# Kernel optimization log

Hardware: AMD Instinct MI355X
Metric: run time of the kernel (lower is better)

The kernel has to match this reference:

```python
import jax, jax.numpy as jnp
import numpy as np

N_NODES = 100000
N_EDGES = 1600000
D = 128
NUM_LAYERS = 3
BN_EPS = 1e-5


def setup_inputs() -> dict:
    key = jax.random.key(0)
    k1, k2, k3 = jax.random.split(key, 3)
    x = jax.random.normal(k1, (N_NODES, D), dtype=jnp.float32)
    edge_index = jax.random.randint(k2, (2, N_EDGES), 0, N_NODES, dtype=jnp.int32)
    # xavier-uniform-ish scale for relu gain
    scale = jnp.sqrt(2.0) * jnp.sqrt(6.0 / (D + D))
    Ws = jax.random.uniform(k3, (NUM_LAYERS, D, D), dtype=jnp.float32, minval=-1.0, maxval=1.0) * scale
    gammas = jnp.ones((NUM_LAYERS - 1, D), dtype=jnp.float32)
    betas = jnp.zeros((NUM_LAYERS - 1, D), dtype=jnp.float32)
    return {"x": x, "edge_index": edge_index, "Ws": Ws, "gammas": gammas, "betas": betas}


def gcn_conv(x, W, src, dst, num_nodes):
    # GCNConv(normalize=False, bias=False): linear then scatter-add aggregation
    h = x @ W                               # [N, D]
    msgs = h[src]                           # [E, D] irregular gather
    return jax.ops.segment_sum(msgs, dst, num_segments=num_nodes)  # [N, D] scatter-add


def batch_norm(x, gamma, beta):
    # training-mode BN over node dim, biased variance (torch semantics), deterministic
    mu = jnp.mean(x, axis=0)
    var = jnp.var(x, axis=0)
    return (x - mu) * jax.lax.rsqrt(var + BN_EPS) * gamma + beta


def reference(x, edge_index, Ws, gammas, betas):
    src, dst = edge_index[0], edge_index[1]
    n = x.shape[0]
    for i in range(NUM_LAYERS):
        x = gcn_conv(x, Ws[i], src, dst, n)
        if i != NUM_LAYERS - 1:
            x = batch_norm(x, gammas[i], betas[i])
            x = jax.nn.relu(x)
            # dropout omitted for a deterministic reference (eval-equivalent)
    return jax.nn.log_softmax(x, axis=-1)
```

## Files before the change

kernel.cpp:

```cpp
#include <hip/hip_runtime.h>

#define BN_EPS 1e-5f

typedef __attribute__((ext_vector_type(8))) short bf16x8;
typedef __attribute__((ext_vector_type(4))) float f32x4;

union VU {
    uint4 u;
    bf16x8 b;
};


__global__ __launch_bounds__(256) void hist_k(const int* __restrict__ dst, int E,
                                              int* __restrict__ ghist, int NB) {
    __shared__ int lh[128];
    if (threadIdx.x < 128) lh[threadIdx.x] = 0;
    __syncthreads();
    for (int i = blockIdx.x * 256 + threadIdx.x; i < E; i += gridDim.x * 256)
        atomicAdd(&lh[dst[i] >> 10], 1);
    __syncthreads();
    if (threadIdx.x < 128 && threadIdx.x < NB && lh[threadIdx.x])
        atomicAdd(&ghist[threadIdx.x * 16], lh[threadIdx.x]);
}

__global__ __launch_bounds__(128) void pscan_k(const int* __restrict__ ghist, int NB,
                                               int* __restrict__ sbase, int* __restrict__ csrB,
                                               int* __restrict__ rowptr, int n, int E) {
    __shared__ int pa[128], pc[128];
    int t = threadIdx.x;
    int v = (t < NB) ? ghist[t * 16] : 0;
    int vp = (v + 15) & ~15;
    pa[t] = vp;
    pc[t] = v;
    __syncthreads();
    for (int s = 1; s < 128; s <<= 1) {
        int ta = (t >= s) ? pa[t - s] : 0;
        int tc = (t >= s) ? pc[t - s] : 0;
        __syncthreads();
        pa[t] += ta;
        pc[t] += tc;
        __syncthreads();
    }
    if (t < NB) {
        sbase[t] = pa[t] - vp;
        csrB[t] = pc[t] - v;
        if (t == NB - 1) {
            csrB[NB] = pc[t];
            rowptr[n] = E;
        }
    }
}

#define CHUNK 2048
__global__ __launch_bounds__(256) void bin_k(const int* __restrict__ src, const int* __restrict__ dst, int E,
                                             const int* __restrict__ sbase, int* __restrict__ snext,
                                             int* __restrict__ staged, int NB) {
    __shared__ int hist[128];
    __shared__ int base[128];
    int t = threadIdx.x;
    int c0 = blockIdx.x * CHUNK;
    if (c0 >= E) return;
    if (t < 128) hist[t] = 0;
    __syncthreads();
    int bk[8], pk[8], rk[8];
#pragma unroll
    for (int k = 0; k < 8; ++k) {
        int i = c0 + k * 256 + t;
        bk[k] = -1;
        if (i < E) {
            int d = dst[i];
            int b = d >> 10;
            bk[k] = b;
            pk[k] = src[i] | ((d & 1023) << 17);
            rk[k] = atomicAdd(&hist[b], 1);
        }
    }
    __syncthreads();
    if (t < NB) base[t] = sbase[t] + atomicAdd(&snext[t * 16], hist[t]);
    __syncthreads();
#pragma unroll
    for (int k = 0; k < 8; ++k)
        if (bk[k] >= 0) staged[base[bk[k]] + rk[k]] = pk[k];
}

__global__ __launch_bounds__(1024) void csr_k(const int* __restrict__ staged, const int* __restrict__ ghist,
                                              const int* __restrict__ sbase, const int* __restrict__ csrB,
                                              int* __restrict__ rowptr, int* __restrict__ ssrc, int n) {
    __shared__ int hist[1024], cur[1024];
    int b = blockIdx.x, t = threadIdx.x;
    int nodeBase = b << 10;
    hist[t] = 0;
    __syncthreads();
    int s0 = sbase[b], c = ghist[b * 16];
    for (int j = t; j < c; j += 1024) atomicAdd(&hist[staged[s0 + j] >> 17], 1);
    __syncthreads();
    int v = hist[t];
    for (int s = 1; s < 1024; s <<= 1) {
        int tv = (t >= s) ? hist[t - s] : 0;
        __syncthreads();
        hist[t] += tv;
        __syncthreads();
    }
    int ex = hist[t] - v;
    int cb = csrB[b];
    if (nodeBase + t < n) rowptr[nodeBase + t] = cb + ex;
    cur[t] = ex;
    __syncthreads();
    for (int j = t; j < c; j += 1024) {
        int e = staged[s0 + j];
        int p = atomicAdd(&cur[e >> 17], 1);
        ssrc[cb + p] = e & 131071;
    }
}


static __device__ __forceinline__ unsigned short f2bf(float f) {
    unsigned u = __float_as_uint(f);
    unsigned r = (u + 0x7FFFu + ((u >> 16) & 1u)) >> 16;
    return (unsigned short)r;
}
static __device__ __forceinline__ float bf_lo(unsigned u) { return __uint_as_float(u << 16); }
static __device__ __forceinline__ float bf_hi(unsigned u) { return __uint_as_float(u & 0xFFFF0000u); }


__global__ __launch_bounds__(256) void prepw_k(const float* __restrict__ Ws, uint4* __restrict__ Wp) {
    int id = blockIdx.x * 256 + threadIdx.x;
    if (id >= 3 * 4 * 8 * 64) return;
    int lane = id & 63;
    int nt = (id >> 6) & 7;
    int kt = (id >> 9) & 3;
    int L = id >> 11;
    int quad = lane >> 4, l16 = lane & 15;
    const float* wsrc = Ws + L * 16384 + (kt * 32 + quad * 8) * 128 + nt * 16 + l16;
    unsigned short s[8];
#pragma unroll
    for (int j = 0; j < 8; ++j) s[j] = f2bf(wsrc[j * 128]);
    uint4 pk;
    pk.x = (unsigned)s[0] | ((unsigned)s[1] << 16);
    pk.y = (unsigned)s[2] | ((unsigned)s[3] << 16);
    pk.z = (unsigned)s[4] | ((unsigned)s[5] << 16);
    pk.w = (unsigned)s[6] | ((unsigned)s[7] << 16);
    Wp[id] = pk;
}


template <int MODE>
__global__ __launch_bounds__(256) void mgemm_k(const float* __restrict__ Xf, const unsigned short* __restrict__ Xb,
                                               const uint4* __restrict__ Wp, unsigned short* __restrict__ H,
                                               const float* __restrict__ ss, int n) {
    int lane = threadIdx.x & 63;
    int quad = lane >> 4, l16 = lane & 15;
    int wid = (blockIdx.x * 256 + threadIdx.x) >> 6;
    int nw = (gridDim.x * 256) >> 6;
    int ntiles = (n + 15) >> 4;

    VU b[4][8];
#pragma unroll
    for (int kt = 0; kt < 4; ++kt)
#pragma unroll
        for (int nt = 0; nt < 8; ++nt) b[kt][nt].u = Wp[(kt * 8 + nt) * 64 + lane];

    auto loadA = [&](int tile, VU* a) {
        int row = tile * 16 + l16;
#pragma unroll
        for (int kt = 0; kt < 4; ++kt) {
            float f[8];
            if (MODE == 0) {
                const float* xr = Xf + (size_t)row * 128 + kt * 32 + quad * 8;
                float4 u0 = *(const float4*)(xr);
                float4 u1 = *(const float4*)(xr + 4);
                f[0] = u0.x; f[1] = u0.y; f[2] = u0.z; f[3] = u0.w;
                f[4] = u1.x; f[5] = u1.y; f[6] = u1.z; f[7] = u1.w;
            } else {
                int sl = kt * 2 + (quad >> 1);
                uint4 u = *(const uint4*)(Xb + ((size_t)sl * n + row) * 16 + (quad & 1) * 8);
                f[0] = bf_lo(u.x); f[1] = bf_hi(u.x); f[2] = bf_lo(u.y); f[3] = bf_hi(u.y);
                f[4] = bf_lo(u.z); f[5] = bf_hi(u.z); f[6] = bf_lo(u.w); f[7] = bf_hi(u.w);
                const float4* scp = (const float4*)(ss + kt * 32 + quad * 8);
                const float4* shp = (const float4*)(ss + 128 + kt * 32 + quad * 8);
                float4 c0 = scp[0], c1 = scp[1], d0 = shp[0], d1 = shp[1];
                f[0] = fmaxf(fmaf(f[0], c0.x, d0.x), 0.f);
                f[1] = fmaxf(fmaf(f[1], c0.y, d0.y), 0.f);
                f[2] = fmaxf(fmaf(f[2], c0.z, d0.z), 0.f);
                f[3] = fmaxf(fmaf(f[3], c0.w, d0.w), 0.f);
                f[4] = fmaxf(fmaf(f[4], c1.x, d1.x), 0.f);
                f[5] = fmaxf(fmaf(f[5], c1.y, d1.y), 0.f);
                f[6] = fmaxf(fmaf(f[6], c1.z, d1.z), 0.f);
                f[7] = fmaxf(fmaf(f[7], c1.w, d1.w), 0.f);
            }
            uint4 pk;
            pk.x = (unsigned)f2bf(f[0]) | ((unsigned)f2bf(f[1]) << 16);
            pk.y = (unsigned)f2bf(f[2]) | ((unsigned)f2bf(f[3]) << 16);
            pk.z = (unsigned)f2bf(f[4]) | ((unsigned)f2bf(f[5]) << 16);
            pk.w = (unsigned)f2bf(f[6]) | ((unsigned)f2bf(f[7]) << 16);
            a[kt].u = pk;
        }
    };

    int t = wid;
    VU a[4];
    if (t < ntiles) loadA(t, a);

    while (t < ntiles) {
        int tn = t + nw;
        VU an[4];
        if (tn < ntiles) loadA(tn, an);

        f32x4 acc[8];
#pragma unroll
        for (int nt = 0; nt < 8; ++nt) acc[nt] = (f32x4){0.f, 0.f, 0.f, 0.f};
#pragma unroll
        for (int kt = 0; kt < 4; ++kt)
#pragma unroll
            for (int nt = 0; nt < 8; ++nt)
                acc[nt] = __builtin_amdgcn_mfma_f32_16x16x32_bf16(b[kt][nt].b, a[kt].b, acc[nt], 0, 0, 0);

        int row = t * 16 + l16;
#pragma unroll
        for (int nt = 0; nt < 8; ++nt) {
            uint2 pk;
            pk.x = (unsigned)f2bf(acc[nt][0]) | ((unsigned)f2bf(acc[nt][1]) << 16);
            pk.y = (unsigned)f2bf(acc[nt][2]) | ((unsigned)f2bf(acc[nt][3]) << 16);
            *(uint2*)(H + ((size_t)nt * n + row) * 16 + quad * 4) = pk;
        }

#pragma unroll
        for (int kt = 0; kt < 4; ++kt) a[kt] = an[kt];
        t = tn;
    }
}


template <int MODE>
__global__ __launch_bounds__(256) void aggs_k(const unsigned short* __restrict__ H, const int* __restrict__ rowptr,
                                              const int* __restrict__ ssrc, unsigned* __restrict__ outb,
                                              float* __restrict__ outf, float* __restrict__ stats, int n) {
    __shared__ float sred[4][4][8];
    int slice = blockIdx.x & 7;
    int bg = blockIdx.x >> 3;
    int lane = threadIdx.x & 63;
    int wv = threadIdx.x >> 6;
    int g = lane >> 3;
    int f = lane & 7;
    int wid = bg * 4 + wv;
    int nwave = (gridDim.x >> 3) * 4;
    const unsigned short* hs = H + (size_t)slice * n * 16 + f * 2;
    float s0 = 0, s1 = 0, q0 = 0, q1 = 0;

    for (int base = wid * 8; base < n; base += nwave * 8) {
        int node = base + g;
        bool valid = node < n;
        int cn = valid ? node : (n - 1);
        int beg = rowptr[cn];
        int end = valid ? rowptr[cn + 1] : beg;
        float ax = 0.f, ay = 0.f;

        for (int s = 0;; s += 16) {
            if (__ballot((beg + s) < end) == 0) break;
            int idx[16];
#pragma unroll
            for (int k = 0; k < 16; ++k) idx[k] = ssrc[beg + s + k];
            unsigned v[16];
#pragma unroll
            for (int k = 0; k < 16; ++k) v[k] = *(const unsigned*)(hs + (size_t)idx[k] * 16);
#pragma unroll
            for (int k = 0; k < 16; ++k) {
                float sc = (beg + s + k < end) ? 1.f : 0.f;
                ax = fmaf(sc, bf_lo(v[k]), ax);
                ay = fmaf(sc, bf_hi(v[k]), ay);
            }
        }

        if (MODE == 0) {
            if (valid) outb[((size_t)slice * n + node) * 8 + f] = (unsigned)f2bf(ax) | ((unsigned)f2bf(ay) << 16);
            s0 += ax; q0 += ax * ax;
            s1 += ay; q1 += ay * ay;
        } else {
            if (valid) *(float2*)(outf + (size_t)node * 128 + slice * 16 + f * 2) = make_float2(ax, ay);
        }
    }

    if (MODE == 0) {
        s0 += __shfl_xor(s0, 8); s0 += __shfl_xor(s0, 16); s0 += __shfl_xor(s0, 32);
        s1 += __shfl_xor(s1, 8); s1 += __shfl_xor(s1, 16); s1 += __shfl_xor(s1, 32);
        q0 += __shfl_xor(q0, 8); q0 += __shfl_xor(q0, 16); q0 += __shfl_xor(q0, 32);
        q1 += __shfl_xor(q1, 8); q1 += __shfl_xor(q1, 16); q1 += __shfl_xor(q1, 32);
        if (g == 0) {
            sred[wv][0][f] = s0;
            sred[wv][1][f] = s1;
            sred[wv][2][f] = q0;
            sred[wv][3][f] = q1;
        }
        __syncthreads();
        if (wv == 0 && g == 0) {
            float t0 = (sred[0][0][f] + sred[1][0][f]) + (sred[2][0][f] + sred[3][0][f]);
            float t1 = (sred[0][1][f] + sred[1][1][f]) + (sred[2][1][f] + sred[3][1][f]);
            float t2 = (sred[0][2][f] + sred[1][2][f]) + (sred[2][2][f] + sred[3][2][f]);
            float t3 = (sred[0][3][f] + sred[1][3][f]) + (sred[2][3][f] + sred[3][3][f]);
            atomicAdd(&stats[slice * 16 + 2 * f], t0);
            atomicAdd(&stats[slice * 16 + 2 * f + 1], t1);
            atomicAdd(&stats[128 + slice * 16 + 2 * f], t2);
            atomicAdd(&stats[128 + slice * 16 + 2 * f + 1], t3);
        }
    }
}


__global__ __launch_bounds__(256) void lsm_k(float* __restrict__ out, int n) {
    int lane = threadIdx.x & 63;
    int wid = (blockIdx.x * 256 + threadIdx.x) >> 6;
    int nw = (gridDim.x * 256) >> 6;
    for (int node = wid; node < n; node += nw) {
        float2 v = *(float2*)(out + (size_t)node * 128 + 2 * lane);
        float m = fmaxf(v.x, v.y);
#pragma unroll
        for (int off = 32; off > 0; off >>= 1) m = fmaxf(m, __shfl_xor(m, off));
        float ex = expf(v.x - m) + expf(v.y - m);
#pragma unroll
        for (int off = 32; off > 0; off >>= 1) ex += __shfl_xor(ex, off);
        float lse = m + logf(ex);
        *(float2*)(out + (size_t)node * 128 + 2 * lane) = make_float2(v.x - lse, v.y - lse);
    }
}


__global__ void bnfin_k(const float* __restrict__ stats, const float* __restrict__ gamma,
                        const float* __restrict__ beta, float* __restrict__ ss, int n) {
    int f = threadIdx.x;
    if (f < 128) {
        float mu = stats[f] / n;
        float var = stats[128 + f] / n - mu * mu;
        float rs = rsqrtf(fmaxf(var, 0.f) + BN_EPS);
        float sc = gamma[f] * rs;
        ss[f] = sc;
        ss[128 + f] = beta[f] - mu * sc;
    }
}


extern "C" void kernel_launch(void* const* d_in, const int* in_sizes, int n_in,
                              void* d_out, int out_size, void* d_ws, size_t ws_size,
                              hipStream_t stream) {
    const float* x = (const float*)d_in[0];
    const int* ei = (const int*)d_in[1];
    const float* Ws = (const float*)d_in[2];
    const float* gammas = (const float*)d_in[3];
    const float* betas = (const float*)d_in[4];
    int N = in_sizes[0] / 128;
    int E = in_sizes[1] / 2;
    const int* src = ei;
    const int* dst = ei + E;
    float* out = (float*)d_out;

    char* w = (char*)d_ws;
    size_t o = 0;
    auto alloc = [&](size_t bytes) { char* p = w + o; o += (bytes + 511) & ~511ull; return p; };
    unsigned short* h = (unsigned short*)alloc((size_t)N * 128 * 2);
    unsigned short* h2 = (unsigned short*)alloc((size_t)N * 128 * 2);
    int* rowptr = (int*)alloc(((size_t)N + 1) * 4);
    int* ssrc = (int*)alloc(((size_t)E + 256) * 4);
    uint4* Wp = (uint4*)alloc(3 * 2048 * 16);
    float* stats = (float*)alloc(512 * 4);
    float* ss = (float*)alloc(512 * 4);

    int NB = (N + 1023) >> 10;
    int* ghist = (int*)alloc((size_t)NB * 16 * 4);
    int* snext = (int*)alloc((size_t)NB * 16 * 4);
    int* sbase = (int*)alloc((size_t)NB * 4);
    int* csrB = (int*)alloc(((size_t)NB + 1) * 4);
    int* staged = (int*)h2;

    hipMemsetAsync(ghist, 0, (size_t)NB * 16 * 4, stream);
    hipMemsetAsync(snext, 0, (size_t)NB * 16 * 4, stream);
    hipMemsetAsync(stats, 0, 512 * 4, stream);
    hipMemsetAsync(ssrc + E, 0, 256 * 4, stream);

    prepw_k<<<24, 256, 0, stream>>>(Ws, Wp);
    hist_k<<<256, 256, 0, stream>>>(dst, E, ghist, NB);
    pscan_k<<<1, 128, 0, stream>>>(ghist, NB, sbase, csrB, rowptr, N, E);
    bin_k<<<(E + CHUNK - 1) / CHUNK, 256, 0, stream>>>(src, dst, E, sbase, snext, staged, NB);
    csr_k<<<NB, 1024, 0, stream>>>(staged, ghist, sbase, csrB, rowptr, ssrc, N);

    const int AGG_BLOCKS = 2048;
    const int GEMM_BLOCKS = 512;

    mgemm_k<0><<<GEMM_BLOCKS, 256, 0, stream>>>(x, nullptr, Wp, h, nullptr, N);
    aggs_k<0><<<AGG_BLOCKS, 256, 0, stream>>>(h, rowptr, ssrc, (unsigned*)h2, nullptr, stats, N);
    bnfin_k<<<1, 128, 0, stream>>>(stats, gammas, betas, ss, N);
    mgemm_k<1><<<GEMM_BLOCKS, 256, 0, stream>>>(nullptr, h2, Wp + 2048, h, ss, N);
    aggs_k<0><<<AGG_BLOCKS, 256, 0, stream>>>(h, rowptr, ssrc, (unsigned*)h2, nullptr, stats + 256, N);
    bnfin_k<<<1, 128, 0, stream>>>(stats + 256, gammas + 128, betas + 128, ss + 256, N);
    mgemm_k<1><<<GEMM_BLOCKS, 256, 0, stream>>>(nullptr, h2, Wp + 4096, h, ss + 256, N);
    aggs_k<1><<<AGG_BLOCKS, 256, 0, stream>>>(h, rowptr, ssrc, nullptr, out, nullptr, N);
    lsm_k<<<2048, 256, 0, stream>>>(out, N);
}
```

Baseline: 584.7 us.

## Switch node features to row-major layout with one wave per node in aggregation

Node features are now stored row-major (node × 128 bf16) instead of in 8 column slices of 16 features, and the GEMM loads and stores are updated to match. The aggregation kernel now gives each wave one whole node: every lane gathers one dword (2 features) per neighbor, so each neighbor fetch reads a full contiguous 256-byte row instead of eight 32-byte slice reads spread over separate passes. Neighbor indices are read once per node rather than once per slice, with the next batch of 8 indices prefetched. In exchange the graph is processed in one pass rather than 8 slice-local passes, so the per-slice cache locality is lost, and the gather depth per loop iteration drops to 8.

```diff
diff --git a/kernel.cpp b/kernel.cpp
--- a/kernel.cpp
+++ b/kernel.cpp
@@ -172,8 +172,7 @@
                 f[0] = u0.x; f[1] = u0.y; f[2] = u0.z; f[3] = u0.w;
                 f[4] = u1.x; f[5] = u1.y; f[6] = u1.z; f[7] = u1.w;
             } else {
-                int sl = kt * 2 + (quad >> 1);
-                uint4 u = *(const uint4*)(Xb + ((size_t)sl * n + row) * 16 + (quad & 1) * 8);
+                uint4 u = *(const uint4*)(Xb + (size_t)row * 128 + kt * 32 + quad * 8);
                 f[0] = bf_lo(u.x); f[1] = bf_hi(u.x); f[2] = bf_lo(u.y); f[3] = bf_hi(u.y);
                 f[4] = bf_lo(u.z); f[5] = bf_hi(u.z); f[6] = bf_lo(u.w); f[7] = bf_hi(u.w);
                 const float4* scp = (const float4*)(ss + kt * 32 + quad * 8);
@@ -221,7 +220,7 @@
             uint2 pk;
             pk.x = (unsigned)f2bf(acc[nt][0]) | ((unsigned)f2bf(acc[nt][1]) << 16);
             pk.y = (unsigned)f2bf(acc[nt][2]) | ((unsigned)f2bf(acc[nt][3]) << 16);
-            *(uint2*)(H + ((size_t)nt * n + row) * 16 + quad * 4) = pk;
+            *(uint2*)(H + (size_t)row * 128 + nt * 16 + quad * 4) = pk;
         }
 
 #pragma unroll
@@ -232,75 +231,67 @@
 
 
 template <int MODE>
-__global__ __launch_bounds__(256) void aggs_k(const unsigned short* __restrict__ H, const int* __restrict__ rowptr,
+__global__ __launch_bounds__(256) void aggr_k(const unsigned* __restrict__ Hdw, const int* __restrict__ rowptr,
                                               const int* __restrict__ ssrc, unsigned* __restrict__ outb,
                                               float* __restrict__ outf, float* __restrict__ stats, int n) {
-    __shared__ float sred[4][4][8];
-    int slice = blockIdx.x & 7;
-    int bg = blockIdx.x >> 3;
+    __shared__ float sred[4][4][64];
     int lane = threadIdx.x & 63;
     int wv = threadIdx.x >> 6;
-    int g = lane >> 3;
-    int f = lane & 7;
-    int wid = bg * 4 + wv;
-    int nwave = (gridDim.x >> 3) * 4;
-    const unsigned short* hs = H + (size_t)slice * n * 16 + f * 2;
-    float s0 = 0, s1 = 0, q0 = 0, q1 = 0;
-
-    for (int base = wid * 8; base < n; base += nwave * 8) {
-        int node = base + g;
-        bool valid = node < n;
-        int cn = valid ? node : (n - 1);
-        int beg = rowptr[cn];
-        int end = valid ? rowptr[cn + 1] : beg;
-        float ax = 0.f, ay = 0.f;
-
-        for (int s = 0;; s += 16) {
-            if (__ballot((beg + s) < end) == 0) break;
-            int idx[16];
-#pragma unroll
-            for (int k = 0; k < 16; ++k) idx[k] = ssrc[beg + s + k];
-            unsigned v[16];
-#pragma unroll
-            for (int k = 0; k < 16; ++k) v[k] = *(const unsigned*)(hs + (size_t)idx[k] * 16);
-#pragma unroll
-            for (int k = 0; k < 16; ++k) {
-                float sc = (beg + s + k < end) ? 1.f : 0.f;
-                ax = fmaf(sc, bf_lo(v[k]), ax);
-                ay = fmaf(sc, bf_hi(v[k]), ay);
+    int wid = blockIdx.x * 4 + wv;
+    int nwave = gridDim.x * 4;
+    float s0 = 0.f, s1 = 0.f, q0 = 0.f, q1 = 0.f;
+
+    for (int node = wid; node < n; node += nwave) {
+        int beg = __builtin_amdgcn_readfirstlane(rowptr[node]);
+        int end = __builtin_amdgcn_readfirstlane(rowptr[node + 1]);
+        int d = end - beg;
+        float a0 = 0.f, a1 = 0.f;
+
+        int idx[8];
+#pragma unroll
+        for (int k = 0; k < 8; ++k) idx[k] = ssrc[beg + k];
+
+        for (int s = 0; s < d; s += 8) {
+            int idn[8];
+#pragma unroll
+            for (int k = 0; k < 8; ++k) idn[k] = ssrc[beg + s + 8 + k];
+            unsigned v[8];
+#pragma unroll
+            for (int k = 0; k < 8; ++k) v[k] = Hdw[(size_t)(unsigned)idx[k] * 64 + lane];
+#pragma unroll
+            for (int k = 0; k < 8; ++k) {
+                float sc = (s + k < d) ? 1.f : 0.f;
+                a0 = fmaf(sc, bf_lo(v[k]), a0);
+                a1 = fmaf(sc, bf_hi(v[k]), a1);
             }
+#pragma unroll
+            for (int k = 0; k < 8; ++k) idx[k] = idn[k];
         }
 
         if (MODE == 0) {
-            if (valid) outb[((size_t)slice * n + node) * 8 + f] = (unsigned)f2bf(ax) | ((unsigned)f2bf(ay) << 16);
-            s0 += ax; q0 += ax * ax;
-            s1 += ay; q1 += ay * ay;
+            outb[(size_t)node * 64 + lane] = (unsigned)f2bf(a0) | ((unsigned)f2bf(a1) << 16);
+            s0 += a0; q0 += a0 * a0;
+            s1 += a1; q1 += a1 * a1;
         } else {
-            if (valid) *(float2*)(outf + (size_t)node * 128 + slice * 16 + f * 2) = make_float2(ax, ay);
+            *(float2*)(outf + (size_t)node * 128 + 2 * lane) = make_float2(a0, a1);
         }
     }
 
     if (MODE == 0) {
-        s0 += __shfl_xor(s0, 8); s0 += __shfl_xor(s0, 16); s0 += __shfl_xor(s0, 32);
-        s1 += __shfl_xor(s1, 8); s1 += __shfl_xor(s1, 16); s1 += __shfl_xor(s1, 32);
-        q0 += __shfl_xor(q0, 8); q0 += __shfl_xor(q0, 16); q0 += __shfl_xor(q0, 32);
-        q1 += __shfl_xor(q1, 8); q1 += __shfl_xor(q1, 16); q1 += __shfl_xor(q1, 32);
-        if (g == 0) {
-            sred[wv][0][f] = s0;
-            sred[wv][1][f] = s1;
-            sred[wv][2][f] = q0;
-            sred[wv][3][f] = q1;
-        }
-        __syncthreads();
-        if (wv == 0 && g == 0) {
-            float t0 = (sred[0][0][f] + sred[1][0][f]) + (sred[2][0][f] + sred[3][0][f]);
-            float t1 = (sred[0][1][f] + sred[1][1][f]) + (sred[2][1][f] + sred[3][1][f]);
-            float t2 = (sred[0][2][f] + sred[1][2][f]) + (sred[2][2][f] + sred[3][2][f]);
-            float t3 = (sred[0][3][f] + sred[1][3][f]) + (sred[2][3][f] + sred[3][3][f]);
-            atomicAdd(&stats[slice * 16 + 2 * f], t0);
-            atomicAdd(&stats[slice * 16 + 2 * f + 1], t1);
-            atomicAdd(&stats[128 + slice * 16 + 2 * f], t2);
-            atomicAdd(&stats[128 + slice * 16 + 2 * f + 1], t3);
+        sred[wv][0][lane] = s0;
+        sred[wv][1][lane] = s1;
+        sred[wv][2][lane] = q0;
+        sred[wv][3][lane] = q1;
+        __syncthreads();
+        if (wv == 0) {
+            float t0 = (sred[0][0][lane] + sred[1][0][lane]) + (sred[2][0][lane] + sred[3][0][lane]);
+            float t1 = (sred[0][1][lane] + sred[1][1][lane]) + (sred[2][1][lane] + sred[3][1][lane]);
+            float t2 = (sred[0][2][lane] + sred[1][2][lane]) + (sred[2][2][lane] + sred[3][2][lane]);
+            float t3 = (sred[0][3][lane] + sred[1][3][lane]) + (sred[2][3][lane] + sred[3][3][lane]);
+            atomicAdd(&stats[2 * lane], t0);
+            atomicAdd(&stats[2 * lane + 1], t1);
+            atomicAdd(&stats[128 + 2 * lane], t2);
+            atomicAdd(&stats[128 + 2 * lane + 1], t3);
         }
     }
 }
@@ -385,12 +376,12 @@
     const int GEMM_BLOCKS = 512;
 
     mgemm_k<0><<<GEMM_BLOCKS, 256, 0, stream>>>(x, nullptr, Wp, h, nullptr, N);
-    aggs_k<0><<<AGG_BLOCKS, 256, 0, stream>>>(h, rowptr, ssrc, (unsigned*)h2, nullptr, stats, N);
+    aggr_k<0><<<AGG_BLOCKS, 256, 0, stream>>>((const unsigned*)h, rowptr, ssrc, (unsigned*)h2, nullptr, stats, N);
     bnfin_k<<<1, 128, 0, stream>>>(stats, gammas, betas, ss, N);
     mgemm_k<1><<<GEMM_BLOCKS, 256, 0, stream>>>(nullptr, h2, Wp + 2048, h, ss, N);
-    aggs_k<0><<<AGG_BLOCKS, 256, 0, stream>>>(h, rowptr, ssrc, (unsigned*)h2, nullptr, stats + 256, N);
+    aggr_k<0><<<AGG_BLOCKS, 256, 0, stream>>>((const unsigned*)h, rowptr, ssrc, (unsigned*)h2, nullptr, stats + 256, N);
     bnfin_k<<<1, 128, 0, stream>>>(stats + 256, gammas + 128, betas + 128, ss + 256, N);
     mgemm_k<1><<<GEMM_BLOCKS, 256, 0, stream>>>(nullptr, h2, Wp + 4096, h, ss + 256, N);
-    aggs_k<1><<<AGG_BLOCKS, 256, 0, stream>>>(h, rowptr, ssrc, nullptr, out, nullptr, N);
+    aggr_k<1><<<AGG_BLOCKS, 256, 0, stream>>>((const unsigned*)h, rowptr, ssrc, nullptr, out, nullptr, N);
     lsm_k<<<2048, 256, 0, stream>>>(out, N);
 }
```

Result: slower. 601.4 us (+2.9%).

## Degree-sort nodes within buckets, software-pipeline gathers, fold memsets into prepw

Applied to the files above, without the earlier changes.

csr_k now counting-sorts each 1024-node bucket by in-degree (capped at 63) and writes an order permutation. The aggregation kernel processes nodes in that order, so the 8 nodes sharing a wave have similar degrees and less divergent padding work. The gather loop now runs a wave-uniform trip count in chunks of 8, with the next chunk's indices prefetched while the current one is summed. The four memsets are folded into prepw_k and the aggregation grid is set to 2000 blocks. The cost is an extra indirection load per node, and rows that read index padding past the last edge rely on the zeroed tail of ssrc.

```diff
diff --git a/kernel.cpp b/kernel.cpp
--- a/kernel.cpp
+++ b/kernel.cpp
@@ -85,11 +85,14 @@
 
 __global__ __launch_bounds__(1024) void csr_k(const int* __restrict__ staged, const int* __restrict__ ghist,
                                               const int* __restrict__ sbase, const int* __restrict__ csrB,
-                                              int* __restrict__ rowptr, int* __restrict__ ssrc, int n) {
+                                              int* __restrict__ rowptr, int* __restrict__ ssrc,
+                                              int* __restrict__ order, int n) {
     __shared__ int hist[1024], cur[1024];
+    __shared__ int dbin[64], dbs[64];
     int b = blockIdx.x, t = threadIdx.x;
     int nodeBase = b << 10;
     hist[t] = 0;
+    if (t < 64) dbin[t] = 0;
     __syncthreads();
     int s0 = sbase[b], c = ghist[b * 16];
     for (int j = t; j < c; j += 1024) atomicAdd(&hist[staged[s0 + j] >> 17], 1);
@@ -103,7 +106,8 @@
     }
     int ex = hist[t] - v;
     int cb = csrB[b];
-    if (nodeBase + t < n) rowptr[nodeBase + t] = cb + ex;
+    bool vn = (nodeBase + t) < n;
+    if (vn) rowptr[nodeBase + t] = cb + ex;
     cur[t] = ex;
     __syncthreads();
     for (int j = t; j < c; j += 1024) {
@@ -111,6 +115,24 @@
         int p = atomicAdd(&cur[e >> 17], 1);
         ssrc[cb + p] = e & 131071;
     }
+    int bin = 0, rk = 0;
+    if (vn) {
+        bin = min(v, 63);
+        rk = atomicAdd(&dbin[bin], 1);
+    }
+    __syncthreads();
+    if (t < 64) {
+        int cc = dbin[t];
+        int x = cc;
+#pragma unroll
+        for (int off = 1; off < 64; off <<= 1) {
+            int y = __shfl_up(x, off);
+            if (t >= off) x += y;
+        }
+        dbs[t] = x - cc;
+    }
+    __syncthreads();
+    if (vn) order[nodeBase + dbs[bin] + rk] = nodeBase + t;
 }
 
 
@@ -123,8 +145,14 @@
 static __device__ __forceinline__ float bf_hi(unsigned u) { return __uint_as_float(u & 0xFFFF0000u); }
 
 
-__global__ __launch_bounds__(256) void prepw_k(const float* __restrict__ Ws, uint4* __restrict__ Wp) {
+__global__ __launch_bounds__(256) void prepw_k(const float* __restrict__ Ws, uint4* __restrict__ Wp,
+                                               int* __restrict__ ghist, int* __restrict__ snext,
+                                               float* __restrict__ stats, int* __restrict__ ssrcPad, int NB16) {
     int id = blockIdx.x * 256 + threadIdx.x;
+    if (id < NB16) ghist[id] = 0;
+    else if (id < 2 * NB16) snext[id - NB16] = 0;
+    else if (id < 2 * NB16 + 512) stats[id - 2 * NB16] = 0.f;
+    else if (id < 2 * NB16 + 512 + 256) ssrcPad[id - 2 * NB16 - 512] = 0;
     if (id >= 3 * 4 * 8 * 64) return;
     int lane = id & 63;
     int nt = (id >> 6) & 7;
@@ -233,8 +261,9 @@
 
 template <int MODE>
 __global__ __launch_bounds__(256) void aggs_k(const unsigned short* __restrict__ H, const int* __restrict__ rowptr,
-                                              const int* __restrict__ ssrc, unsigned* __restrict__ outb,
-                                              float* __restrict__ outf, float* __restrict__ stats, int n) {
+                                              const int* __restrict__ ssrc, const int* __restrict__ order,
+                                              unsigned* __restrict__ outb, float* __restrict__ outf,
+                                              float* __restrict__ stats, int n) {
     __shared__ float sred[4][4][8];
     int slice = blockIdx.x & 7;
     int bg = blockIdx.x >> 3;
@@ -248,27 +277,39 @@
     float s0 = 0, s1 = 0, q0 = 0, q1 = 0;
 
     for (int base = wid * 8; base < n; base += nwave * 8) {
-        int node = base + g;
-        bool valid = node < n;
-        int cn = valid ? node : (n - 1);
-        int beg = rowptr[cn];
-        int end = valid ? rowptr[cn + 1] : beg;
+        bool valid = (base + g) < n;
+        int node = valid ? order[base + g] : 0;
+        int beg = rowptr[node];
+        int end = valid ? rowptr[node + 1] : beg;
         float ax = 0.f, ay = 0.f;
 
-        for (int s = 0;; s += 16) {
-            if (__ballot((beg + s) < end) == 0) break;
-            int idx[16];
-#pragma unroll
-            for (int k = 0; k < 16; ++k) idx[k] = ssrc[beg + s + k];
-            unsigned v[16];
-#pragma unroll
-            for (int k = 0; k < 16; ++k) v[k] = *(const unsigned*)(hs + (size_t)idx[k] * 16);
-#pragma unroll
-            for (int k = 0; k < 16; ++k) {
-                float sc = (beg + s + k < end) ? 1.f : 0.f;
+        int md = end - beg;
+        md = max(md, __shfl_xor(md, 8));
+        md = max(md, __shfl_xor(md, 16));
+        md = max(md, __shfl_xor(md, 32));
+        int nb = (md + 7) >> 3;
+
+        int idx[8];
+#pragma unroll
+        for (int k = 0; k < 8; ++k) idx[k] = ssrc[beg + k];
+
+        int j0 = beg;
+        for (int it = 0; it < nb; ++it) {
+            unsigned v[8];
+#pragma unroll
+            for (int k = 0; k < 8; ++k) v[k] = *(const unsigned*)(hs + (size_t)(unsigned)idx[k] * 16);
+            int idn[8];
+#pragma unroll
+            for (int k = 0; k < 8; ++k) idn[k] = ssrc[j0 + 8 + k];
+#pragma unroll
+            for (int k = 0; k < 8; ++k) {
+                float sc = (j0 + k < end) ? 1.f : 0.f;
                 ax = fmaf(sc, bf_lo(v[k]), ax);
                 ay = fmaf(sc, bf_hi(v[k]), ay);
             }
+#pragma unroll
+            for (int k = 0; k < 8; ++k) idx[k] = idn[k];
+            j0 += 8;
         }
 
         if (MODE == 0) {
@@ -359,6 +400,7 @@
     unsigned short* h2 = (unsigned short*)alloc((size_t)N * 128 * 2);
     int* rowptr = (int*)alloc(((size_t)N + 1) * 4);
     int* ssrc = (int*)alloc(((size_t)E + 256) * 4);
+    int* order = (int*)alloc((size_t)N * 4);
     uint4* Wp = (uint4*)alloc(3 * 2048 * 16);
     float* stats = (float*)alloc(512 * 4);
     float* ss = (float*)alloc(512 * 4);
@@ -370,27 +412,22 @@
     int* csrB = (int*)alloc(((size_t)NB + 1) * 4);
     int* staged = (int*)h2;
 
-    hipMemsetAsync(ghist, 0, (size_t)NB * 16 * 4, stream);
-    hipMemsetAsync(snext, 0, (size_t)NB * 16 * 4, stream);
-    hipMemsetAsync(stats, 0, 512 * 4, stream);
-    hipMemsetAsync(ssrc + E, 0, 256 * 4, stream);
-
-    prepw_k<<<24, 256, 0, stream>>>(Ws, Wp);
+    prepw_k<<<24, 256, 0, stream>>>(Ws, Wp, ghist, snext, stats, ssrc + E, NB * 16);
     hist_k<<<256, 256, 0, stream>>>(dst, E, ghist, NB);
     pscan_k<<<1, 128, 0, stream>>>(ghist, NB, sbase, csrB, rowptr, N, E);
     bin_k<<<(E + CHUNK - 1) / CHUNK, 256, 0, stream>>>(src, dst, E, sbase, snext, staged, NB);
-    csr_k<<<NB, 1024, 0, stream>>>(staged, ghist, sbase, csrB, rowptr, ssrc, N);
-
-    const int AGG_BLOCKS = 2048;
+    csr_k<<<NB, 1024, 0, stream>>>(staged, ghist, sbase, csrB, rowptr, ssrc, order, N);
+
+    const int AGG_BLOCKS = 2000;
     const int GEMM_BLOCKS = 512;
 
     mgemm_k<0><<<GEMM_BLOCKS, 256, 0, stream>>>(x, nullptr, Wp, h, nullptr, N);
-    aggs_k<0><<<AGG_BLOCKS, 256, 0, stream>>>(h, rowptr, ssrc, (unsigned*)h2, nullptr, stats, N);
+    aggs_k<0><<<AGG_BLOCKS, 256, 0, stream>>>(h, rowptr, ssrc, order, (unsigned*)h2, nullptr, stats, N);
     bnfin_k<<<1, 128, 0, stream>>>(stats, gammas, betas, ss, N);
     mgemm_k<1><<<GEMM_BLOCKS, 256, 0, stream>>>(nullptr, h2, Wp + 2048, h, ss, N);
-    aggs_k<0><<<AGG_BLOCKS, 256, 0, stream>>>(h, rowptr, ssrc, (unsigned*)h2, nullptr, stats + 256, N);
+    aggs_k<0><<<AGG_BLOCKS, 256, 0, stream>>>(h, rowptr, ssrc, order, (unsigned*)h2, nullptr, stats + 256, N);
     bnfin_k<<<1, 128, 0, stream>>>(stats + 256, gammas + 128, betas + 128, ss + 256, N);
     mgemm_k<1><<<GEMM_BLOCKS, 256, 0, stream>>>(nullptr, h2, Wp + 4096, h, ss + 256, N);
-    aggs_k<1><<<AGG_BLOCKS, 256, 0, stream>>>(h, rowptr, ssrc, nullptr, out, nullptr, N);
+    aggs_k<1><<<AGG_BLOCKS, 256, 0, stream>>>(h, rowptr, ssrc, order, nullptr, out, nullptr, N);
     lsm_k<<<2048, 256, 0, stream>>>(out, N);
 }
```

Result: faster. 561.1 us (-4.0%).

## Pipeline aggregation index loads, pad H with zero row, fold memsets into prep kernel

Applied to the files above, without the earlier changes.

The aggregation inner loop now processes edges in batches of 8, prefetching the next batch's source indices while gathering the current rows. Out-of-range edges point to a padded zero row at index n, which removes the per-edge masking multiply. The H buffers gain 16 padding rows and a node-stride parameter. The four memset calls are folded into the weight-prep kernel to cut launch overhead. The per-group max-degree reduction changes the loop trip count, so uneven degrees within a group may waste gathers.

```diff
diff --git a/kernel.cpp b/kernel.cpp
--- a/kernel.cpp
+++ b/kernel.cpp
@@ -123,8 +123,19 @@
 static __device__ __forceinline__ float bf_hi(unsigned u) { return __uint_as_float(u & 0xFFFF0000u); }
 
 
-__global__ __launch_bounds__(256) void prepw_k(const float* __restrict__ Ws, uint4* __restrict__ Wp) {
+__global__ __launch_bounds__(256) void prepw_k(const float* __restrict__ Ws, uint4* __restrict__ Wp,
+                                               int* __restrict__ ghist, int* __restrict__ snext,
+                                               float* __restrict__ stats, int* __restrict__ ssrcPad,
+                                               unsigned short* __restrict__ h, int NB16, int n, int np) {
     int id = blockIdx.x * 256 + threadIdx.x;
+    if (id < NB16) ghist[id] = 0;
+    else if (id < 2 * NB16) snext[id - NB16] = 0;
+    else if (id < 2 * NB16 + 512) stats[id - 2 * NB16] = 0.f;
+    else if (id < 2 * NB16 + 512 + 256) ssrcPad[id - 2 * NB16 - 512] = 0;
+    if (id >= 4096 && id < 4096 + 128) {
+        int sl = (id - 4096) >> 4, ft = (id - 4096) & 15;
+        h[((size_t)sl * np + n) * 16 + ft] = 0;
+    }
     if (id >= 3 * 4 * 8 * 64) return;
     int lane = id & 63;
     int nt = (id >> 6) & 7;
@@ -147,7 +158,7 @@
 template <int MODE>
 __global__ __launch_bounds__(256) void mgemm_k(const float* __restrict__ Xf, const unsigned short* __restrict__ Xb,
                                                const uint4* __restrict__ Wp, unsigned short* __restrict__ H,
-                                               const float* __restrict__ ss, int n) {
+                                               const float* __restrict__ ss, int n, int np) {
     int lane = threadIdx.x & 63;
     int quad = lane >> 4, l16 = lane & 15;
     int wid = (blockIdx.x * 256 + threadIdx.x) >> 6;
@@ -173,7 +184,7 @@
                 f[4] = u1.x; f[5] = u1.y; f[6] = u1.z; f[7] = u1.w;
             } else {
                 int sl = kt * 2 + (quad >> 1);
-                uint4 u = *(const uint4*)(Xb + ((size_t)sl * n + row) * 16 + (quad & 1) * 8);
+                uint4 u = *(const uint4*)(Xb + ((size_t)sl * np + row) * 16 + (quad & 1) * 8);
                 f[0] = bf_lo(u.x); f[1] = bf_hi(u.x); f[2] = bf_lo(u.y); f[3] = bf_hi(u.y);
                 f[4] = bf_lo(u.z); f[5] = bf_hi(u.z); f[6] = bf_lo(u.w); f[7] = bf_hi(u.w);
                 const float4* scp = (const float4*)(ss + kt * 32 + quad * 8);
@@ -221,7 +232,7 @@
             uint2 pk;
             pk.x = (unsigned)f2bf(acc[nt][0]) | ((unsigned)f2bf(acc[nt][1]) << 16);
             pk.y = (unsigned)f2bf(acc[nt][2]) | ((unsigned)f2bf(acc[nt][3]) << 16);
-            *(uint2*)(H + ((size_t)nt * n + row) * 16 + quad * 4) = pk;
+            *(uint2*)(H + ((size_t)nt * np + row) * 16 + quad * 4) = pk;
         }
 
 #pragma unroll
@@ -234,7 +245,7 @@
 template <int MODE>
 __global__ __launch_bounds__(256) void aggs_k(const unsigned short* __restrict__ H, const int* __restrict__ rowptr,
                                               const int* __restrict__ ssrc, unsigned* __restrict__ outb,
-                                              float* __restrict__ outf, float* __restrict__ stats, int n) {
+                                              float* __restrict__ outf, float* __restrict__ stats, int n, int np) {
     __shared__ float sred[4][4][8];
     int slice = blockIdx.x & 7;
     int bg = blockIdx.x >> 3;
@@ -244,7 +255,7 @@
     int f = lane & 7;
     int wid = bg * 4 + wv;
     int nwave = (gridDim.x >> 3) * 4;
-    const unsigned short* hs = H + (size_t)slice * n * 16 + f * 2;
+    const unsigned short* hs = H + (size_t)slice * np * 16 + f * 2;
     float s0 = 0, s1 = 0, q0 = 0, q1 = 0;
 
     for (int base = wid * 8; base < n; base += nwave * 8) {
@@ -255,24 +266,42 @@
         int end = valid ? rowptr[cn + 1] : beg;
         float ax = 0.f, ay = 0.f;
 
-        for (int s = 0;; s += 16) {
-            if (__ballot((beg + s) < end) == 0) break;
-            int idx[16];
-#pragma unroll
-            for (int k = 0; k < 16; ++k) idx[k] = ssrc[beg + s + k];
-            unsigned v[16];
-#pragma unroll
-            for (int k = 0; k < 16; ++k) v[k] = *(const unsigned*)(hs + (size_t)idx[k] * 16);
-#pragma unroll
-            for (int k = 0; k < 16; ++k) {
-                float sc = (beg + s + k < end) ? 1.f : 0.f;
-                ax = fmaf(sc, bf_lo(v[k]), ax);
-                ay = fmaf(sc, bf_hi(v[k]), ay);
+        int md = end - beg;
+        md = max(md, __shfl_xor(md, 8));
+        md = max(md, __shfl_xor(md, 16));
+        md = max(md, __shfl_xor(md, 32));
+        int nb = (md + 7) >> 3;
+
+        int idx[8];
+#pragma unroll
+        for (int k = 0; k < 8; ++k) {
+            int j = beg + k;
+            idx[k] = (j < end) ? ssrc[j] : n;
+        }
+
+        int j0 = beg;
+        for (int it = 0; it < nb; ++it) {
+            unsigned v[8];
+#pragma unroll
+            for (int k = 0; k < 8; ++k) v[k] = *(const unsigned*)(hs + (size_t)(unsigned)idx[k] * 16);
+            int idn[8];
+#pragma unroll
+            for (int k = 0; k < 8; ++k) {
+                int j = j0 + 8 + k;
+                idn[k] = (j < end) ? ssrc[j] : n;
             }
+#pragma unroll
+            for (int k = 0; k < 8; ++k) {
+                ax += bf_lo(v[k]);
+                ay += bf_hi(v[k]);
+            }
+#pragma unroll
+            for (int k = 0; k < 8; ++k) idx[k] = idn[k];
+            j0 += 8;
         }
 
         if (MODE == 0) {
-            if (valid) outb[((size_t)slice * n + node) * 8 + f] = (unsigned)f2bf(ax) | ((unsigned)f2bf(ay) << 16);
+            if (valid) outb[((size_t)slice * np + node) * 8 + f] = (unsigned)f2bf(ax) | ((unsigned)f2bf(ay) << 16);
             s0 += ax; q0 += ax * ax;
             s1 += ay; q1 += ay * ay;
         } else {
@@ -351,12 +380,13 @@
     const int* src = ei;
     const int* dst = ei + E;
     float* out = (float*)d_out;
+    int NP = N + 16;
 
     char* w = (char*)d_ws;
     size_t o = 0;
     auto alloc = [&](size_t bytes) { char* p = w + o; o += (bytes + 511) & ~511ull; return p; };
-    unsigned short* h = (unsigned short*)alloc((size_t)N * 128 * 2);
-    unsigned short* h2 = (unsigned short*)alloc((size_t)N * 128 * 2);
+    unsigned short* h = (unsigned short*)alloc((size_t)NP * 128 * 2);
+    unsigned short* h2 = (unsigned short*)alloc((size_t)NP * 128 * 2);
     int* rowptr = (int*)alloc(((size_t)N + 1) * 4);
     int* ssrc = (int*)alloc(((size_t)E + 256) * 4);
     uint4* Wp = (uint4*)alloc(3 * 2048 * 16);
@@ -370,12 +400,7 @@
     int* csrB = (int*)alloc(((size_t)NB + 1) * 4);
     int* staged = (int*)h2;
 
-    hipMemsetAsync(ghist, 0, (size_t)NB * 16 * 4, stream);
-    hipMemsetAsync(snext, 0, (size_t)NB * 16 * 4, stream);
-    hipMemsetAsync(stats, 0, 512 * 4, stream);
-    hipMemsetAsync(ssrc + E, 0, 256 * 4, stream);
-
-    prepw_k<<<24, 256, 0, stream>>>(Ws, Wp);
+    prepw_k<<<24, 256, 0, stream>>>(Ws, Wp, ghist, snext, stats, ssrc + E, h, NB * 16, N, NP);
     hist_k<<<256, 256, 0, stream>>>(dst, E, ghist, NB);
     pscan_k<<<1, 128, 0, stream>>>(ghist, NB, sbase, csrB, rowptr, N, E);
     bin_k<<<(E + CHUNK - 1) / CHUNK, 256, 0, stream>>>(src, dst, E, sbase, snext, staged, NB);
@@ -384,13 +409,13 @@
     const int AGG_BLOCKS = 2048;
     const int GEMM_BLOCKS = 512;
 
-    mgemm_k<0><<<GEMM_BLOCKS, 256, 0, stream>>>(x, nullptr, Wp, h, nullptr, N);
-    aggs_k<0><<<AGG_BLOCKS, 256, 0, stream>>>(h, rowptr, ssrc, (unsigned*)h2, nullptr, stats, N);
+    mgemm_k<0><<<GEMM_BLOCKS, 256, 0, stream>>>(x, nullptr, Wp, h, nullptr, N, NP);
+    aggs_k<0><<<AGG_BLOCKS, 256, 0, stream>>>(h, rowptr, ssrc, (unsigned*)h2, nullptr, stats, N, NP);
     bnfin_k<<<1, 128, 0, stream>>>(stats, gammas, betas, ss, N);
-    mgemm_k<1><<<GEMM_BLOCKS, 256, 0, stream>>>(nullptr, h2, Wp + 2048, h, ss, N);
-    aggs_k<0><<<AGG_BLOCKS, 256, 0, stream>>>(h, rowptr, ssrc, (unsigned*)h2, nullptr, stats + 256, N);
+    mgemm_k<1><<<GEMM_BLOCKS, 256, 0, stream>>>(nullptr, h2, Wp + 2048, h, ss, N, NP);
+    aggs_k<0><<<AGG_BLOCKS, 256, 0, stream>>>(h, rowptr, ssrc, (unsigned*)h2, nullptr, stats + 256, N, NP);
     bnfin_k<<<1, 128, 0, stream>>>(stats + 256, gammas + 128, betas + 128, ss + 256, N);
-    mgemm_k<1><<<GEMM_BLOCKS, 256, 0, stream>>>(nullptr, h2, Wp + 4096, h, ss + 256, N);
-    aggs_k<1><<<AGG_BLOCKS, 256, 0, stream>>>(h, rowptr, ssrc, nullptr, out, nullptr, N);
+    mgemm_k<1><<<GEMM_BLOCKS, 256, 0, stream>>>(nullptr, h2, Wp + 4096, h, ss + 256, N, NP);
+    aggs_k<1><<<AGG_BLOCKS, 256, 0, stream>>>(h, rowptr, ssrc, nullptr, out, nullptr, N, NP);
     lsm_k<<<2048, 256, 0, stream>>>(out, N);
 }
```

New measurement: 481.7 us (median of 3 runs). 17.6% less time.
